# Kernel optimization log

Measured on AMD Instinct MI355X. Metric: run time of the kernel, lower is better.

Reference implementation:

```python
import jax, jax.numpy as jnp
import numpy as np

B, S, D = 4, 2048, 1024
H = 16
HD = D // H  # 64


def setup_inputs() -> dict:
    key = jax.random.key(0)
    kx, kq, kp = jax.random.split(key, 3)
    x = jax.random.normal(kx, (B, S, D), dtype=jnp.float32)
    # torch Linear weights are [out, in]; match init scale ~ U(-1/sqrt(in), 1/sqrt(in))
    lim = 1.0 / np.sqrt(D)
    w_qkv = jax.random.uniform(kq, (3 * D, D), dtype=jnp.float32, minval=-lim, maxval=lim)
    w_proj = jax.random.uniform(kp, (D, D), dtype=jnp.float32, minval=-lim, maxval=lim)
    return {"x": x, "w_qkv": w_qkv, "w_proj": w_proj}


def reference(x, w_qkv, w_proj):
    b, s, d = x.shape
    qkv = jnp.einsum('bsd,ed->bse', x, w_qkv)  # [B,S,3D]
    q, k, v = jnp.split(qkv, 3, axis=-1)
    # [B,H,S,HD]
    q = q.reshape(b, s, H, HD).transpose(0, 2, 1, 3)
    k = k.reshape(b, s, H, HD).transpose(0, 2, 1, 3)
    v = v.reshape(b, s, H, HD).transpose(0, 2, 1, 3)
    scale = 1.0 / np.sqrt(HD)
    attn = jnp.einsum('bhqd,bhkd->bhqk', q, k) * scale  # [B,H,S,S]
    causal = jnp.tril(jnp.ones((s, s), dtype=bool))
    attn = jnp.where(causal[None, None], attn, -jnp.inf)
    attn = jax.nn.softmax(attn, axis=-1)
    out = jnp.einsum('bhqk,bhkd->bhqd', attn, v)
    out = out.transpose(0, 2, 1, 3).reshape(b, s, d)
    return jnp.einsum('bsd,ed->bse', out, w_proj)
```

## Files before the change

### kernel.cpp

```cpp
#include <hip/hip_runtime.h>

typedef unsigned short u16;
typedef unsigned int u32;

#define B_ 4
#define S_ 2048
#define D_ 1024
#define H_ 16
#define HD_ 64
#define M_ (B_ * S_)
#define QK_ (2 * D_)

typedef __bf16 bf16x8 __attribute__((ext_vector_type(8)));
typedef float f32x4 __attribute__((ext_vector_type(4)));

#define MASKVAL (-1.0e30f)
#define RESCALE_THR 8.0f

static __device__ __forceinline__ u16 f2bf_hw(float f) {
    union { __bf16 b; u16 u; } v;
    v.b = (__bf16)f;
    return v.u;
}

static __device__ __forceinline__ void gload16(const u16* g, u16* l) {
    __builtin_amdgcn_global_load_lds(
        (const __attribute__((address_space(1))) void*)g,
        (__attribute__((address_space(3))) void*)l, 16, 0, 0);
}

__global__ __launch_bounds__(256) void cvt_bf16(const float* __restrict__ src,
                                                u16* __restrict__ dst) {
    size_t i = ((size_t)blockIdx.x * 256 + threadIdx.x) * 8;
    float4 a = *(const float4*)(src + i);
    float4 b = *(const float4*)(src + i + 4);
    union { u16 h[8]; int4 v; } pk;
    pk.h[0] = f2bf_hw(a.x); pk.h[1] = f2bf_hw(a.y);
    pk.h[2] = f2bf_hw(a.z); pk.h[3] = f2bf_hw(a.w);
    pk.h[4] = f2bf_hw(b.x); pk.h[5] = f2bf_hw(b.y);
    pk.h[6] = f2bf_hw(b.z); pk.h[7] = f2bf_hw(b.w);
    *(int4*)(dst + i) = pk.v;
}

template <int EPI>
__global__ __launch_bounds__(256) void gemm_bb(const u16* __restrict__ A,
                                               const u16* __restrict__ Bw,
                                               void* __restrict__ Cout,
                                               int Ndim, int Kdim) {
    __shared__ u16 Alds[128 * 64];
    __shared__ u16 Blds[128 * 64];
    const int t = threadIdx.x;
    const int bx = blockIdx.x, by = blockIdx.y;
    const int wave = t >> 6, lane = t & 63;
    const int ml = lane & 15, quad = lane >> 4;
    const int wm = (wave >> 1) * 64, wn = (wave & 1) * 64;
    const int rowA0 = by * 128, rowB0 = bx * 128;
    const int sr8 = lane >> 3;
    const int sc8 = (lane & 7) * 8;

    f32x4 acc[4][4];
    const f32x4 zero = {0.f, 0.f, 0.f, 0.f};
#pragma unroll
    for (int i = 0; i < 4; ++i)
#pragma unroll
        for (int j = 0; j < 4; ++j) acc[i][j] = zero;

    for (int k0 = 0; k0 < Kdim; k0 += 64) {
        __syncthreads();
#pragma unroll
        for (int p = 0; p < 4; ++p) {
            const int rbase = wave * 32 + p * 8;
            gload16(&A[(size_t)(rowA0 + rbase + sr8) * Kdim + k0 + sc8],
                    &Alds[rbase * 64]);
            gload16(&Bw[(size_t)(rowB0 + rbase + sr8) * Kdim + k0 + sc8],
                    &Blds[rbase * 64]);
        }
        __syncthreads();
#pragma unroll
        for (int kc = 0; kc < 2; ++kc) {
            bf16x8 a[4], b[4];
#pragma unroll
            for (int i = 0; i < 4; ++i)
                a[i] = *(const bf16x8*)(&Alds[(wm + i * 16 + ml) * 64 + kc * 32 + quad * 8]);
#pragma unroll
            for (int j = 0; j < 4; ++j)
                b[j] = *(const bf16x8*)(&Blds[(wn + j * 16 + ml) * 64 + kc * 32 + quad * 8]);
#pragma unroll
            for (int i = 0; i < 4; ++i)
#pragma unroll
                for (int j = 0; j < 4; ++j)
                    acc[i][j] = __builtin_amdgcn_mfma_f32_16x16x32_bf16(a[i], b[j], acc[i][j], 0, 0, 0);
        }
    }

    if constexpr (EPI == 0) {
        u16* C = (u16*)Cout;
#pragma unroll
        for (int i = 0; i < 4; ++i)
#pragma unroll
            for (int j = 0; j < 4; ++j)
#pragma unroll
                for (int r = 0; r < 4; ++r) {
                    int row = rowA0 + wm + i * 16 + quad * 4 + r;
                    int col = rowB0 + wn + j * 16 + ml;
                    C[(size_t)row * Ndim + col] = f2bf_hw(acc[i][j][r]);
                }
    } else if constexpr (EPI == 1) {
        u16* Vt = (u16*)Cout;
#pragma unroll
        for (int i = 0; i < 4; ++i)
#pragma unroll
            for (int j = 0; j < 4; ++j) {
                int row0 = rowA0 + wm + i * 16 + quad * 4;
                int col = rowB0 + wn + j * 16 + ml;
                int b = row0 >> 11;
                int s0 = row0 & (S_ - 1);
                union { u16 h[4]; ushort4 v; } pk;
#pragma unroll
                for (int r = 0; r < 4; ++r) pk.h[r] = f2bf_hw(acc[i][j][r]);
                *(ushort4*)(&Vt[((size_t)(b * D_ + col)) * S_ + s0]) = pk.v;
            }
    } else {
        float* C = (float*)Cout;
#pragma unroll
        for (int i = 0; i < 4; ++i)
#pragma unroll
            for (int j = 0; j < 4; ++j)
#pragma unroll
                for (int r = 0; r < 4; ++r) {
                    int row = rowA0 + wm + i * 16 + quad * 4 + r;
                    int col = rowB0 + wn + j * 16 + ml;
                    C[(size_t)row * Ndim + col] = acc[i][j][r];
                }
    }
}

__global__ __launch_bounds__(256, 2) void attn2(const u16* __restrict__ qk,
                                                const u16* __restrict__ Vt,
                                                u16* __restrict__ AO) {
    __shared__ u16 Klds[2][64 * 64];
    __shared__ u16 Vlds[2][64 * 64];
    __shared__ u16 Plds[4][32 * 68];
    const int t = threadIdx.x;
    const int wave = t >> 6, lane = t & 63;
    const int ml = lane & 15, quad = lane >> 4;
    const int j = blockIdx.x >> 6;
    const int bh = blockIdx.x & 63;
    const int b = bh >> 4, h = bh & 15;
    const size_t rowbase = (size_t)b * S_;

    const int srow8 = lane >> 3;
    const int schunk = ((lane & 7) ^ srow8) * 8;

    int qw[2], ktw[2];
    qw[0] = j * 128 + wave * 32;
    qw[1] = (15 - j) * 128 + wave * 32;
    ktw[0] = (qw[0] + 31) >> 6;
    ktw[1] = (qw[1] + 31) >> 6;
    const int ktmax = ((15 - j) * 128 + 127) >> 6;

    bf16x8 qf[2][2][2];
#pragma unroll
    for (int T = 0; T < 2; ++T)
#pragma unroll
        for (int mi = 0; mi < 2; ++mi)
#pragma unroll
            for (int kc = 0; kc < 2; ++kc) {
                bf16x8 q = *(const bf16x8*)(&qk[(rowbase + qw[T] + mi * 16 + ml) * QK_ +
                                                h * HD_ + kc * 32 + quad * 8]);
#pragma unroll
                for (int e = 0; e < 8; ++e) {
                    float f = (float)q[e] * 0.125f;
                    q[e] = (__bf16)f;
                }
                qf[T][mi][kc] = q;
            }

    f32x4 o[2][2][4];
    float m[2][2][4], ls[2][2][4];
    const f32x4 zero = {0.f, 0.f, 0.f, 0.f};
#pragma unroll
    for (int T = 0; T < 2; ++T)
#pragma unroll
        for (int mi = 0; mi < 2; ++mi) {
#pragma unroll
            for (int nd = 0; nd < 4; ++nd) o[T][mi][nd] = zero;
#pragma unroll
            for (int r = 0; r < 4; ++r) { m[T][mi][r] = MASKVAL; ls[T][mi][r] = 0.f; }
        }

    auto STAGE = [&](int buf, int kt) {
        const int kb = kt * 64;
#pragma unroll
        for (int p = 0; p < 2; ++p) {
            const int rbase = wave * 16 + p * 8;
            gload16(&qk[(rowbase + kb + rbase + srow8) * QK_ + D_ + h * HD_ + schunk],
                    &Klds[buf][rbase * 64]);
            gload16(&Vt[(size_t)(bh * HD_ + rbase + srow8) * S_ + kb + schunk],
                    &Vlds[buf][rbase * 64]);
        }
    };

    STAGE(0, 0);

    for (int kt = 0; kt <= ktmax; ++kt) {
        const int cur = kt & 1;
        if (kt < ktmax) {
            STAGE(cur ^ 1, kt + 1);
            asm volatile("s_waitcnt vmcnt(4)" ::: "memory");
        } else {
            asm volatile("s_waitcnt vmcnt(0)" ::: "memory");
        }
        __builtin_amdgcn_s_barrier();

        if (kt <= ktw[1]) {
            const int kb = kt * 64;
            bf16x8 kf[4][2], vf[4][2];
#pragma unroll
            for (int ni = 0; ni < 4; ++ni)
#pragma unroll
                for (int kc = 0; kc < 2; ++kc) {
                    const int row = ni * 16 + ml;
                    const int sw = ((kc * 4 + quad) ^ (ml & 7)) * 8;
                    kf[ni][kc] = *(const bf16x8*)(&Klds[cur][row * 64 + sw]);
                    vf[ni][kc] = *(const bf16x8*)(&Vlds[cur][row * 64 + sw]);
                }

#pragma unroll
            for (int T = 0; T < 2; ++T) {
                if (kt > ktw[T]) continue;
                const int qT = qw[T];
                f32x4 sc[2][4];
                __builtin_amdgcn_s_setprio(1);
#pragma unroll
                for (int mi = 0; mi < 2; ++mi)
#pragma unroll
                    for (int ni = 0; ni < 4; ++ni) {
                        f32x4 s = zero;
#pragma unroll
                        for (int kc = 0; kc < 2; ++kc)
                            s = __builtin_amdgcn_mfma_f32_16x16x32_bf16(qf[T][mi][kc], kf[ni][kc], s, 0, 0, 0);
                        sc[mi][ni] = s;
                    }
                __builtin_amdgcn_s_setprio(0);
                if (kb + 63 > qT) {
#pragma unroll
                    for (int mi = 0; mi < 2; ++mi)
#pragma unroll
                        for (int ni = 0; ni < 4; ++ni)
#pragma unroll
                            for (int r = 0; r < 4; ++r) {
                                int q = qT + mi * 16 + quad * 4 + r;
                                int k = kb + ni * 16 + ml;
                                if (k > q) sc[mi][ni][r] = MASKVAL;
                            }
                }
#pragma unroll
                for (int mi = 0; mi < 2; ++mi) {
                    float tm[4];
#pragma unroll
                    for (int r = 0; r < 4; ++r)
                        tm[r] = fmaxf(fmaxf(sc[mi][0][r], sc[mi][1][r]),
                                      fmaxf(sc[mi][2][r], sc[mi][3][r]));
#pragma unroll
                    for (int off = 1; off <= 8; off <<= 1)
#pragma unroll
                        for (int r = 0; r < 4; ++r)
                            tm[r] = fmaxf(tm[r], __shfl_xor(tm[r], off, 64));
                    bool need = false;
#pragma unroll
                    for (int r = 0; r < 4; ++r) need |= (tm[r] > m[T][mi][r] + RESCALE_THR);
                    if (__any(need)) {
                        float al[4];
#pragma unroll
                        for (int r = 0; r < 4; ++r) {
                            float mn = fmaxf(m[T][mi][r], tm[r]);
                            al[r] = __expf(m[T][mi][r] - mn);
                            m[T][mi][r] = mn;
                        }
#pragma unroll
                        for (int r = 0; r < 4; ++r) ls[T][mi][r] *= al[r];
#pragma unroll
                        for (int nd = 0; nd < 4; ++nd)
#pragma unroll
                            for (int r = 0; r < 4; ++r) o[T][mi][nd][r] *= al[r];
                    }
#pragma unroll
                    for (int ni = 0; ni < 4; ++ni)
#pragma unroll
                        for (int r = 0; r < 4; ++r)
                            sc[mi][ni][r] = __expf(sc[mi][ni][r] - m[T][mi][r]);
#pragma unroll
                    for (int r = 0; r < 4; ++r)
                        ls[T][mi][r] += (sc[mi][0][r] + sc[mi][1][r]) + (sc[mi][2][r] + sc[mi][3][r]);
#pragma unroll
                    for (int ni = 0; ni < 4; ++ni)
#pragma unroll
                        for (int r = 0; r < 4; ++r)
                            Plds[wave][(mi * 16 + quad * 4 + r) * 68 + ni * 16 + ml] =
                                f2bf_hw(sc[mi][ni][r]);
                }
                asm volatile("s_waitcnt lgkmcnt(0)" ::: "memory");
                bf16x8 pf[2][2];
#pragma unroll
                for (int mi = 0; mi < 2; ++mi)
#pragma unroll
                    for (int kc = 0; kc < 2; ++kc)
                        pf[mi][kc] = *(const bf16x8*)(&Plds[wave][(mi * 16 + ml) * 68 + kc * 32 + quad * 8]);
                __builtin_amdgcn_s_setprio(1);
#pragma unroll
                for (int mi = 0; mi < 2; ++mi)
#pragma unroll
                    for (int nd = 0; nd < 4; ++nd)
#pragma unroll
                        for (int kc = 0; kc < 2; ++kc)
                            o[T][mi][nd] = __builtin_amdgcn_mfma_f32_16x16x32_bf16(pf[mi][kc], vf[nd][kc],
                                                                                   o[T][mi][nd], 0, 0, 0);
                __builtin_amdgcn_s_setprio(0);
            }
        }
        __builtin_amdgcn_s_barrier();
    }

#pragma unroll
    for (int T = 0; T < 2; ++T)
#pragma unroll
        for (int mi = 0; mi < 2; ++mi) {
            float s4[4], rl[4];
#pragma unroll
            for (int r = 0; r < 4; ++r) s4[r] = ls[T][mi][r];
#pragma unroll
            for (int off = 1; off <= 8; off <<= 1)
#pragma unroll
                for (int r = 0; r < 4; ++r) s4[r] += __shfl_xor(s4[r], off, 64);
#pragma unroll
            for (int r = 0; r < 4; ++r) rl[r] = 1.0f / s4[r];
#pragma unroll
            for (int nd = 0; nd < 4; ++nd)
#pragma unroll
                for (int r = 0; r < 4; ++r) {
                    int srow = qw[T] + mi * 16 + quad * 4 + r;
                    AO[(rowbase + srow) * D_ + h * HD_ + nd * 16 + ml] =
                        f2bf_hw(o[T][mi][nd][r] * rl[r]);
                }
        }
}

__global__ __launch_bounds__(256) void copy16(const int4* __restrict__ src,
                                              int4* __restrict__ dst) {
    size_t i = (size_t)blockIdx.x * 256 + threadIdx.x;
    dst[i] = src[i];
}

extern "C" void kernel_launch(void* const* d_in, const int* in_sizes, int n_in,
                              void* d_out, int out_size, void* d_ws, size_t ws_size,
                              hipStream_t stream) {
    const float* x = (const float*)d_in[0];
    const float* wqkv = (const float*)d_in[1];
    const float* wproj = (const float*)d_in[2];
    float* out = (float*)d_out;

    u16* qkw = (u16*)d_ws;
    u16* Vtw = qkw + (size_t)M_ * QK_;

    u16* xb = (u16*)d_out;
    u16* wprojb = xb + (size_t)M_ * D_;
    u16* wqkvb = wprojb + (size_t)D_ * D_;

    const size_t need = ((size_t)M_ * QK_ + 8388608  + (size_t)M_ * D_  +
                         (size_t)D_ * D_ ) * sizeof(u16);
    const bool bigws = ws_size >= need;
    u16* AOb    = bigws ? (Vtw + (size_t)8388608) : xb;
    u16* wprojd = bigws ? (AOb + (size_t)M_ * D_) : wprojb;
    u16* AOp    = bigws ? AOb : qkw;
    u16* wprojp = bigws ? wprojd : qkw + (size_t)M_ * D_;

    cvt_bf16<<<dim3(M_ * D_ / 2048), 256, 0, stream>>>(x, xb);
    cvt_bf16<<<dim3(D_ * D_ / 2048), 256, 0, stream>>>(wproj, wprojd);
    cvt_bf16<<<dim3(3 * D_ * D_ / 2048), 256, 0, stream>>>(wqkv, wqkvb);

    gemm_bb<0><<<dim3(QK_ / 128, M_ / 128), 256, 0, stream>>>(xb, wqkvb, qkw, QK_, D_);
    gemm_bb<1><<<dim3(D_ / 128, M_ / 128), 256, 0, stream>>>(
        xb, wqkvb + (size_t)QK_ * D_, Vtw, D_, D_);
    attn2<<<dim3(512), 256, 0, stream>>>(qkw, Vtw, AOb);
    if (!bigws) {
        copy16<<<dim3((unsigned)(((size_t)M_ * D_ + (size_t)D_ * D_) * 2 / (256 * 16))),
                 256, 0, stream>>>((const int4*)AOb, (int4*)qkw);
    }
    gemm_bb<2><<<dim3(D_ / 128, M_ / 128), 256, 0, stream>>>(AOp, wprojp, out, D_, D_);
}
```

Measured before the change: 303.1 us.

## Split paired causal attention tiles into separate blocks with transposed score layout

The attention kernel no longer pairs a light and a heavy query tile per block. It launches 1024 blocks that each own one 128-row query tile, ordered heavy-first to balance load, and raises the occupancy hint to 3 blocks per CU. S is computed as K·Q^T so each lane holds one query row, which makes the row max and sum reductions cheaper; the P tile is written to LDS with an XOR swizzle. The trade-off is that K/V tiles are reloaded per block instead of shared across the pair, and there is extra shuffle work to broadcast the rescale factors.

```diff
diff --git a/kernel.cpp b/kernel.cpp
--- a/kernel.cpp
+++ b/kernel.cpp
@@ -135,59 +135,54 @@
     }
 }
 
-__global__ __launch_bounds__(256, 2) void attn2(const u16* __restrict__ qk,
+__global__ __launch_bounds__(256, 3) void attn3(const u16* __restrict__ qk,
                                                 const u16* __restrict__ Vt,
                                                 u16* __restrict__ AO) {
     __shared__ u16 Klds[2][64 * 64];
     __shared__ u16 Vlds[2][64 * 64];
-    __shared__ u16 Plds[4][32 * 68];
+    __shared__ u32 Pw[4][32 * 32];
     const int t = threadIdx.x;
     const int wave = t >> 6, lane = t & 63;
     const int ml = lane & 15, quad = lane >> 4;
-    const int j = blockIdx.x >> 6;
+
+    const int jj = blockIdx.x >> 6;
     const int bh = blockIdx.x & 63;
+    const int t4 = jj >> 2, r4 = jj & 3;
+    const int j = (t4 < 2) ? (15 - 4 * t4 - r4) : (12 - 4 * t4 + r4);
     const int b = bh >> 4, h = bh & 15;
     const size_t rowbase = (size_t)b * S_;
 
     const int srow8 = lane >> 3;
     const int schunk = ((lane & 7) ^ srow8) * 8;
 
-    int qw[2], ktw[2];
-    qw[0] = j * 128 + wave * 32;
-    qw[1] = (15 - j) * 128 + wave * 32;
-    ktw[0] = (qw[0] + 31) >> 6;
-    ktw[1] = (qw[1] + 31) >> 6;
-    const int ktmax = ((15 - j) * 128 + 127) >> 6;
-
-    bf16x8 qf[2][2][2];
-#pragma unroll
-    for (int T = 0; T < 2; ++T)
-#pragma unroll
-        for (int mi = 0; mi < 2; ++mi)
-#pragma unroll
-            for (int kc = 0; kc < 2; ++kc) {
-                bf16x8 q = *(const bf16x8*)(&qk[(rowbase + qw[T] + mi * 16 + ml) * QK_ +
-                                                h * HD_ + kc * 32 + quad * 8]);
-#pragma unroll
-                for (int e = 0; e < 8; ++e) {
-                    float f = (float)q[e] * 0.125f;
-                    q[e] = (__bf16)f;
-                }
-                qf[T][mi][kc] = q;
-            }
-
-    f32x4 o[2][2][4];
-    float m[2][2][4], ls[2][2][4];
+    const int qj0 = j * 128 + wave * 32;
+    const int ktw = 2 * j + (wave >> 1);
+    const int ktmax = 2 * j + 1;
+
+    bf16x8 qf[2][2];
+#pragma unroll
+    for (int mi = 0; mi < 2; ++mi)
+#pragma unroll
+        for (int kc = 0; kc < 2; ++kc) {
+            bf16x8 q = *(const bf16x8*)(&qk[(rowbase + qj0 + mi * 16 + ml) * QK_ +
+                                            h * HD_ + kc * 32 + quad * 8]);
+#pragma unroll
+            for (int e = 0; e < 8; ++e) {
+                float f = (float)q[e] * 0.125f;
+                q[e] = (__bf16)f;
+            }
+            qf[mi][kc] = q;
+        }
+
+    f32x4 o[2][4];
+    float m[2], ls[2];
     const f32x4 zero = {0.f, 0.f, 0.f, 0.f};
 #pragma unroll
-    for (int T = 0; T < 2; ++T)
-#pragma unroll
-        for (int mi = 0; mi < 2; ++mi) {
-#pragma unroll
-            for (int nd = 0; nd < 4; ++nd) o[T][mi][nd] = zero;
-#pragma unroll
-            for (int r = 0; r < 4; ++r) { m[T][mi][r] = MASKVAL; ls[T][mi][r] = 0.f; }
-        }
+    for (int mi = 0; mi < 2; ++mi) {
+#pragma unroll
+        for (int nd = 0; nd < 4; ++nd) o[mi][nd] = zero;
+        m[mi] = MASKVAL; ls[mi] = 0.f;
+    }
 
     auto STAGE = [&](int buf, int kt) {
         const int kb = kt * 64;
@@ -213,7 +208,7 @@
         }
         __builtin_amdgcn_s_barrier();
 
-        if (kt <= ktw[1]) {
+        if (kt <= ktw) {
             const int kb = kt * 64;
             bf16x8 kf[4][2], vf[4][2];
 #pragma unroll
@@ -226,124 +221,122 @@
                     vf[ni][kc] = *(const bf16x8*)(&Vlds[cur][row * 64 + sw]);
                 }
 
-#pragma unroll
-            for (int T = 0; T < 2; ++T) {
-                if (kt > ktw[T]) continue;
-                const int qT = qw[T];
-                f32x4 sc[2][4];
-                __builtin_amdgcn_s_setprio(1);
-#pragma unroll
-                for (int mi = 0; mi < 2; ++mi)
-#pragma unroll
-                    for (int ni = 0; ni < 4; ++ni) {
-                        f32x4 s = zero;
-#pragma unroll
-                        for (int kc = 0; kc < 2; ++kc)
-                            s = __builtin_amdgcn_mfma_f32_16x16x32_bf16(qf[T][mi][kc], kf[ni][kc], s, 0, 0, 0);
-                        sc[mi][ni] = s;
+            f32x4 sc[2][4];
+            __builtin_amdgcn_s_setprio(1);
+#pragma unroll
+            for (int mi = 0; mi < 2; ++mi)
+#pragma unroll
+                for (int ni = 0; ni < 4; ++ni) {
+                    f32x4 s = zero;
+#pragma unroll
+                    for (int kc = 0; kc < 2; ++kc)
+                        s = __builtin_amdgcn_mfma_f32_16x16x32_bf16(kf[ni][kc], qf[mi][kc], s, 0, 0, 0);
+                    sc[mi][ni] = s;
+                }
+            __builtin_amdgcn_s_setprio(0);
+
+            if (kb + 63 > qj0) {
+#pragma unroll
+                for (int mi = 0; mi < 2; ++mi) {
+                    const int q = qj0 + mi * 16 + ml;
+#pragma unroll
+                    for (int ni = 0; ni < 4; ++ni)
+#pragma unroll
+                        for (int r = 0; r < 4; ++r) {
+                            int k = kb + ni * 16 + quad * 4 + r;
+                            if (k > q) sc[mi][ni][r] = MASKVAL;
+                        }
+                }
+            }
+
+#pragma unroll
+            for (int mi = 0; mi < 2; ++mi) {
+                float tm = sc[mi][0][0];
+#pragma unroll
+                for (int ni = 0; ni < 4; ++ni)
+#pragma unroll
+                    for (int r = 0; r < 4; ++r) tm = fmaxf(tm, sc[mi][ni][r]);
+                tm = fmaxf(tm, __shfl_xor(tm, 16, 64));
+                tm = fmaxf(tm, __shfl_xor(tm, 32, 64));
+                if (__any(tm > m[mi] + RESCALE_THR)) {
+                    float mn = fmaxf(m[mi], tm);
+                    float al = __expf(m[mi] - mn);
+                    m[mi] = mn;
+                    ls[mi] *= al;
+                    float alr[4];
+#pragma unroll
+                    for (int r = 0; r < 4; ++r)
+                        alr[r] = __shfl(al, (lane & 48) + ((lane & 48) >> 2) + r, 64);
+#pragma unroll
+                    for (int nd = 0; nd < 4; ++nd)
+#pragma unroll
+                        for (int r = 0; r < 4; ++r) o[mi][nd][r] *= alr[r];
+                }
+                float sum = 0.f;
+#pragma unroll
+                for (int ni = 0; ni < 4; ++ni)
+#pragma unroll
+                    for (int r = 0; r < 4; ++r) {
+                        float e = __expf(sc[mi][ni][r] - m[mi]);
+                        sc[mi][ni][r] = e;
+                        sum += e;
                     }
-                __builtin_amdgcn_s_setprio(0);
-                if (kb + 63 > qT) {
-#pragma unroll
-                    for (int mi = 0; mi < 2; ++mi)
-#pragma unroll
-                        for (int ni = 0; ni < 4; ++ni)
-#pragma unroll
-                            for (int r = 0; r < 4; ++r) {
-                                int q = qT + mi * 16 + quad * 4 + r;
-                                int k = kb + ni * 16 + ml;
-                                if (k > q) sc[mi][ni][r] = MASKVAL;
-                            }
-                }
-#pragma unroll
-                for (int mi = 0; mi < 2; ++mi) {
-                    float tm[4];
-#pragma unroll
-                    for (int r = 0; r < 4; ++r)
-                        tm[r] = fmaxf(fmaxf(sc[mi][0][r], sc[mi][1][r]),
-                                      fmaxf(sc[mi][2][r], sc[mi][3][r]));
-#pragma unroll
-                    for (int off = 1; off <= 8; off <<= 1)
-#pragma unroll
-                        for (int r = 0; r < 4; ++r)
-                            tm[r] = fmaxf(tm[r], __shfl_xor(tm[r], off, 64));
-                    bool need = false;
-#pragma unroll
-                    for (int r = 0; r < 4; ++r) need |= (tm[r] > m[T][mi][r] + RESCALE_THR);
-                    if (__any(need)) {
-                        float al[4];
-#pragma unroll
-                        for (int r = 0; r < 4; ++r) {
-                            float mn = fmaxf(m[T][mi][r], tm[r]);
-                            al[r] = __expf(m[T][mi][r] - mn);
-                            m[T][mi][r] = mn;
-                        }
-#pragma unroll
-                        for (int r = 0; r < 4; ++r) ls[T][mi][r] *= al[r];
-#pragma unroll
-                        for (int nd = 0; nd < 4; ++nd)
-#pragma unroll
-                            for (int r = 0; r < 4; ++r) o[T][mi][nd][r] *= al[r];
-                    }
-#pragma unroll
-                    for (int ni = 0; ni < 4; ++ni)
-#pragma unroll
-                        for (int r = 0; r < 4; ++r)
-                            sc[mi][ni][r] = __expf(sc[mi][ni][r] - m[T][mi][r]);
-#pragma unroll
-                    for (int r = 0; r < 4; ++r)
-                        ls[T][mi][r] += (sc[mi][0][r] + sc[mi][1][r]) + (sc[mi][2][r] + sc[mi][3][r]);
-#pragma unroll
-                    for (int ni = 0; ni < 4; ++ni)
-#pragma unroll
-                        for (int r = 0; r < 4; ++r)
-                            Plds[wave][(mi * 16 + quad * 4 + r) * 68 + ni * 16 + ml] =
-                                f2bf_hw(sc[mi][ni][r]);
-                }
-                asm volatile("s_waitcnt lgkmcnt(0)" ::: "memory");
-                bf16x8 pf[2][2];
-#pragma unroll
-                for (int mi = 0; mi < 2; ++mi)
+                ls[mi] += sum;
+#pragma unroll
+                for (int ni = 0; ni < 4; ++ni) {
+                    union { u16 h[4]; ushort4 v; } pk;
+#pragma unroll
+                    for (int r = 0; r < 4; ++r) pk.h[r] = f2bf_hw(sc[mi][ni][r]);
+                    const int row = mi * 16 + ml;
+                    const int word = row * 32 +
+                                     (((ni * 2 + (quad >> 1)) ^ (ml & 7)) << 2) +
+                                     ((quad & 1) * 2);
+                    *(ushort4*)(&Pw[wave][word]) = pk.v;
+                }
+            }
+            asm volatile("s_waitcnt lgkmcnt(0)" ::: "memory");
+            bf16x8 pf[2][2];
+#pragma unroll
+            for (int mi = 0; mi < 2; ++mi)
+#pragma unroll
+                for (int kc = 0; kc < 2; ++kc) {
+                    const int row = mi * 16 + ml;
+                    const int word = row * 32 + ((((kc * 4 + quad)) ^ (ml & 7)) << 2);
+                    pf[mi][kc] = *(const bf16x8*)(&Pw[wave][word]);
+                }
+            __builtin_amdgcn_s_setprio(1);
+#pragma unroll
+            for (int mi = 0; mi < 2; ++mi)
+#pragma unroll
+                for (int nd = 0; nd < 4; ++nd)
 #pragma unroll
                     for (int kc = 0; kc < 2; ++kc)
-                        pf[mi][kc] = *(const bf16x8*)(&Plds[wave][(mi * 16 + ml) * 68 + kc * 32 + quad * 8]);
-                __builtin_amdgcn_s_setprio(1);
-#pragma unroll
-                for (int mi = 0; mi < 2; ++mi)
-#pragma unroll
-                    for (int nd = 0; nd < 4; ++nd)
-#pragma unroll
-                        for (int kc = 0; kc < 2; ++kc)
-                            o[T][mi][nd] = __builtin_amdgcn_mfma_f32_16x16x32_bf16(pf[mi][kc], vf[nd][kc],
-                                                                                   o[T][mi][nd], 0, 0, 0);
-                __builtin_amdgcn_s_setprio(0);
-            }
+                        o[mi][nd] = __builtin_amdgcn_mfma_f32_16x16x32_bf16(pf[mi][kc], vf[nd][kc],
+                                                                            o[mi][nd], 0, 0, 0);
+            __builtin_amdgcn_s_setprio(0);
         }
         __builtin_amdgcn_s_barrier();
     }
 
 #pragma unroll
-    for (int T = 0; T < 2; ++T)
-#pragma unroll
-        for (int mi = 0; mi < 2; ++mi) {
-            float s4[4], rl[4];
-#pragma unroll
-            for (int r = 0; r < 4; ++r) s4[r] = ls[T][mi][r];
-#pragma unroll
-            for (int off = 1; off <= 8; off <<= 1)
-#pragma unroll
-                for (int r = 0; r < 4; ++r) s4[r] += __shfl_xor(s4[r], off, 64);
-#pragma unroll
-            for (int r = 0; r < 4; ++r) rl[r] = 1.0f / s4[r];
-#pragma unroll
-            for (int nd = 0; nd < 4; ++nd)
-#pragma unroll
-                for (int r = 0; r < 4; ++r) {
-                    int srow = qw[T] + mi * 16 + quad * 4 + r;
-                    AO[(rowbase + srow) * D_ + h * HD_ + nd * 16 + ml] =
-                        f2bf_hw(o[T][mi][nd][r] * rl[r]);
-                }
-        }
+    for (int mi = 0; mi < 2; ++mi) {
+        float s = ls[mi];
+        s += __shfl_xor(s, 16, 64);
+        s += __shfl_xor(s, 32, 64);
+        float rl = 1.0f / s;
+        float rlr[4];
+#pragma unroll
+        for (int r = 0; r < 4; ++r)
+            rlr[r] = __shfl(rl, (lane & 48) + ((lane & 48) >> 2) + r, 64);
+#pragma unroll
+        for (int nd = 0; nd < 4; ++nd)
+#pragma unroll
+            for (int r = 0; r < 4; ++r) {
+                int srow = qj0 + mi * 16 + quad * 4 + r;
+                AO[(rowbase + srow) * D_ + h * HD_ + nd * 16 + ml] =
+                    f2bf_hw(o[mi][nd][r] * rlr[r]);
+            }
+    }
 }
 
 __global__ __launch_bounds__(256) void copy16(const int4* __restrict__ src,
@@ -382,7 +375,7 @@
     gemm_bb<0><<<dim3(QK_ / 128, M_ / 128), 256, 0, stream>>>(xb, wqkvb, qkw, QK_, D_);
     gemm_bb<1><<<dim3(D_ / 128, M_ / 128), 256, 0, stream>>>(
         xb, wqkvb + (size_t)QK_ * D_, Vtw, D_, D_);
-    attn2<<<dim3(512), 256, 0, stream>>>(qkw, Vtw, AOb);
+    attn3<<<dim3(1024), 256, 0, stream>>>(qkw, Vtw, AOb);
     if (!bigws) {
         copy16<<<dim3((unsigned)(((size_t)M_ * D_ + (size_t)D_ * D_) * 2 / (256 * 16))),
                  256, 0, stream>>>((const int4*)AOb, (int4*)qkw);
```

After: 269.1 us. -11.2%, faster.
